# Kernel tuning notes

Hardware: AMD Instinct MI355X
Metric: run time of the kernel (lower is better)

Reference implementation:

```python
import jax, jax.numpy as jnp
import numpy as np

N_NODES = 50000
N_EDGES = 800000
IN_DIM = 256
HID = 128


def setup_inputs() -> dict:
    key = jax.random.key(0)
    ks = jax.random.split(key, 8)
    x = jax.random.normal(ks[0], (N_NODES, IN_DIM), dtype=jnp.float32)
    edge_index = jax.random.randint(ks[1], (2, N_EDGES), 0, N_NODES, dtype=jnp.int32)
    edge_weight = jax.random.uniform(ks[2], (N_EDGES,), dtype=jnp.float32)
    # xavier_normal with gain=1.414 as in torch init
    g = 1.414
    W1 = jax.random.normal(ks[3], (HID, IN_DIM), dtype=jnp.float32) * (g * np.sqrt(2.0 / (HID + IN_DIM)))
    W2 = jax.random.normal(ks[4], (HID, HID), dtype=jnp.float32) * (g * np.sqrt(2.0 / (HID + HID)))
    b1 = jnp.zeros((HID,), dtype=jnp.float32)
    b2 = jnp.zeros((HID,), dtype=jnp.float32)
    a1 = jnp.full((1,), 0.25, dtype=jnp.float32)  # nn.PReLU() default init
    a2 = jnp.full((1,), 0.25, dtype=jnp.float32)
    return {"x": x, "edge_index": edge_index, "edge_weight": edge_weight,
            "W1": W1, "b1": b1, "a1": a1, "W2": W2, "b2": b2, "a2": a2}


def _gcn_layer(z, W, b, a, src, dst, w):
    # linear (no bias): [N, out]
    fts = z @ W.T
    # spmm: out[dst] += w * fts[src]
    msg = fts[src] * w[:, None]                      # [E, out]
    out = jax.ops.segment_sum(msg, dst, num_segments=N_NODES) + b
    # PReLU (single shared parameter)
    return jnp.where(out >= 0, out, a * out)


def reference(x, edge_index, edge_weight, W1, b1, a1, W2, b2, a2):
    src, dst = edge_index[0], edge_index[1]
    z = _gcn_layer(x, W1, b1, a1, src, dst, edge_weight)
    z = _gcn_layer(z, W2, b2, a2, src, dst, edge_weight)
    return z
```

## Files before the change

kernel.cpp:

```cpp
#include <hip/hip_runtime.h>

#define HID 128
#define BSH 6
#define BSZ 64
#define NBMAX 1024

typedef unsigned int uint;
typedef unsigned short ushort;
typedef __attribute__((ext_vector_type(8))) short short8;
typedef __attribute__((ext_vector_type(4))) float f32x4;

__device__ __forceinline__ uint pack_bf16x2(float a, float b) {
    uint ua = __float_as_uint(a);
    ua += 0x7fffu + ((ua >> 16) & 1u);
    uint ub = __float_as_uint(b);
    ub += 0x7fffu + ((ub >> 16) & 1u);
    return (ua >> 16) | (ub & 0xffff0000u);
}

__device__ __forceinline__ ushort bf16_of(float x) {
    uint u = __float_as_uint(x);
    u += 0x7fffu + ((u >> 16) & 1u);
    return (ushort)(u >> 16);
}

__device__ __forceinline__ float4 addbias_prelu(float4 v, float4 b, float a) {
    v.x += b.x; v.y += b.y; v.z += b.z; v.w += b.w;
    v.x = v.x >= 0.f ? v.x : a * v.x;
    v.y = v.y >= 0.f ? v.y : a * v.y;
    v.z = v.z >= 0.f ? v.z : a * v.z;
    v.w = v.w >= 0.f ? v.w : a * v.w;
    return v;
}

union FragAB { uint4 u; short8 s; };

__global__ void w_to_frags(const float* __restrict__ W, ushort* __restrict__ Wb, int K) {
    int t = blockIdx.x * 256 + threadIdx.x;
    int total = (K / 32) * 8 * 64;
    if (t >= total) return;
    int lane = t & 63, f = t >> 6;
    int s = f >> 3, c = f & 7;
    int m = c * 16 + (lane & 15);
    int k0 = s * 32 + (lane >> 4) * 8;
    const float* wr = W + (size_t)m * K + k0;
    float4 a = *(const float4*)wr;
    float4 b = *(const float4*)(wr + 4);
    uint4 o = make_uint4(pack_bf16x2(a.x, a.y), pack_bf16x2(a.z, a.w),
                         pack_bf16x2(b.x, b.y), pack_bf16x2(b.z, b.w));
    *(uint4*)(Wb + (size_t)t * 8) = o;
}

template <int K, bool FUSE>
__global__ __launch_bounds__(256) void gemm_mfma(
    const float* __restrict__ X, const ushort* __restrict__ Wb,
    const float* __restrict__ bias, const float* __restrict__ alpha,
    ushort* __restrict__ out, int N) {
    const int lane = threadIdx.x & 63;
    const int wid  = threadIdx.x >> 6;
    const int n0   = blockIdx.x * 64 + wid * 16;
    const int arow = n0 + (lane & 15);
    const bool okA = arow < N;
    const int kgrp = (lane >> 4) * 8;
    const float* xrow = X + (size_t)arow * K;
    const float a_ = FUSE ? alpha[0] : 0.f;

    f32x4 acc[8];
#pragma unroll
    for (int c = 0; c < 8; ++c) acc[c] = (f32x4){0.f, 0.f, 0.f, 0.f};

#pragma unroll
    for (int s = 0; s < K / 32; ++s) {
        const int k0 = s * 32 + kgrp;
        float4 va = make_float4(0.f, 0.f, 0.f, 0.f), vb = va;
        if (okA) {
            va = *(const float4*)(xrow + k0);
            vb = *(const float4*)(xrow + k0 + 4);
        }
        if (FUSE) {
            float4 ba = *(const float4*)(bias + k0);
            float4 bb = *(const float4*)(bias + k0 + 4);
            va = addbias_prelu(va, ba, a_);
            vb = addbias_prelu(vb, bb, a_);
        }
        FragAB af;
        af.u = make_uint4(pack_bf16x2(va.x, va.y), pack_bf16x2(va.z, va.w),
                          pack_bf16x2(vb.x, vb.y), pack_bf16x2(vb.z, vb.w));
#pragma unroll
        for (int c = 0; c < 8; ++c) {
            FragAB bfr;
            bfr.u = *(const uint4*)(Wb + (size_t)((s * 8 + c) * 64 + lane) * 8);
            acc[c] = __builtin_amdgcn_mfma_f32_16x16x32_bf16(af.s, bfr.s, acc[c], 0, 0, 0);
        }
    }
    const int col = lane & 15;
    const int rbase = n0 + (lane >> 4) * 4;
#pragma unroll
    for (int c = 0; c < 8; ++c) {
#pragma unroll
        for (int r = 0; r < 4; ++r) {
            int n = rbase + r;
            if (n < N) out[(size_t)n * HID + c * 16 + col] = bf16_of(acc[c][r]);
        }
    }
}

__global__ __launch_bounds__(256) void bucket_hist(const int* __restrict__ dst,
                                                   int* __restrict__ ghist, int E, int NB) {
    __shared__ int h[NBMAX];
    for (int i = threadIdx.x; i < NB; i += 256) h[i] = 0;
    __syncthreads();
    int stride = gridDim.x * 256;
    for (int e = blockIdx.x * 256 + threadIdx.x; e < E; e += stride)
        atomicAdd(&h[dst[e] >> BSH], 1);
    __syncthreads();
    for (int i = threadIdx.x; i < NB; i += 256) {
        int c = h[i];
        if (c) atomicAdd(&ghist[i], c);
    }
}

__global__ __launch_bounds__(NBMAX) void bucket_scan(const int* __restrict__ ghist,
                                                     int* __restrict__ gbase,
                                                     int* __restrict__ gcur, int NB, int E) {
    __shared__ int l[NBMAX];
    int t = threadIdx.x;
    int v = (t < NB) ? ghist[t] : 0;
    l[t] = v;
    __syncthreads();
    int x = v;
    for (int o = 1; o < NBMAX; o <<= 1) {
        int y = (t >= o) ? l[t - o] : 0;
        __syncthreads();
        x += y;
        l[t] = x;
        __syncthreads();
    }
    if (t < NB) { gbase[t] = x - v; gcur[t] = x - v; }
    if (t == 0) gbase[NB] = E;
}

__global__ __launch_bounds__(256) void bucket_stage(
    const int* __restrict__ src, const int* __restrict__ dst,
    const float* __restrict__ w, int* __restrict__ gcur,
    int2* __restrict__ staged, int E, int NB) {
    __shared__ int lh[NBMAX], lb[NBMAX];
    for (int i = threadIdx.x; i < NB; i += 256) lh[i] = 0;
    __syncthreads();
    int chunk = (E + gridDim.x - 1) / gridDim.x;
    int c0 = blockIdx.x * chunk;
    int c1 = min(c0 + chunk, E);
    for (int e = c0 + threadIdx.x; e < c1; e += 256)
        atomicAdd(&lh[dst[e] >> BSH], 1);
    __syncthreads();
    for (int i = threadIdx.x; i < NB; i += 256) {
        int c = lh[i];
        lb[i] = c ? atomicAdd(&gcur[i], c) : 0;
        lh[i] = 0;
    }
    __syncthreads();
    for (int e = c0 + threadIdx.x; e < c1; e += 256) {
        int d = dst[e];
        int b = d >> BSH;
        int slot = lb[b] + atomicAdd(&lh[b], 1);
        staged[slot] = make_int2(src[e] | ((d & (BSZ - 1)) << 16), __float_as_int(w[e]));
    }
}

__global__ __launch_bounds__(256) void node_sort(
    const int* __restrict__ gbase, const int2* __restrict__ staged,
    int2* __restrict__ csr, int* __restrict__ off, int N) {
    __shared__ int hist[BSZ];
    __shared__ int cur[BSZ];
    const int b = blockIdx.x;
    const int s0 = gbase[b], s1 = gbase[b + 1];
    const int t = threadIdx.x;
    if (t < BSZ) hist[t] = 0;
    __syncthreads();
    for (int e = s0 + t; e < s1; e += 256)
        atomicAdd(&hist[(staged[e].x >> 16) & (BSZ - 1)], 1);
    __syncthreads();
    if (t < BSZ) {
        int x = hist[t];
        int incl = x;
#pragma unroll
        for (int o = 1; o < BSZ; o <<= 1) {
            int y = __shfl_up(incl, o, BSZ);
            if (t >= o) incl += y;
        }
        int excl = incl - x;
        cur[t] = excl;
        int n = (b << BSH) + t;
        if (n <= N) off[n] = s0 + excl;
    }
    __syncthreads();
    for (int e = s0 + t; e < s1; e += 256) {
        int2 m = staged[e];
        int d = (m.x >> 16) & (BSZ - 1);
        int p = atomicAdd(&cur[d], 1);
        csr[s0 + p] = m;
    }
}

__global__ __launch_bounds__(256) void csr_gather_bf16(
    const int* __restrict__ off, const int2* __restrict__ edges,
    const ushort* __restrict__ fts, float* __restrict__ out,
    const float* __restrict__ bias, const float* __restrict__ alpha, int N) {
    int d = blockIdx.x * 4 + (threadIdx.x >> 6);
    if (d >= N) return;
    int lane = threadIdx.x & 63;
    int p = off[d], end = off[d + 1];
    float acc0 = 0.f, acc1 = 0.f;

#define ROWU(e) (*((const uint*)(fts + (size_t)((e).x & 0xffff) * HID) + lane))
#define LO(r) __uint_as_float((r) << 16)
#define HI(r) __uint_as_float((r) & 0xffff0000u)

    for (; p + 3 < end; p += 4) {
        int2 e0 = edges[p], e1 = edges[p + 1], e2 = edges[p + 2], e3 = edges[p + 3];
        uint r0 = ROWU(e0), r1 = ROWU(e1), r2 = ROWU(e2), r3 = ROWU(e3);
        float w0 = __int_as_float(e0.y), w1 = __int_as_float(e1.y);
        float w2 = __int_as_float(e2.y), w3 = __int_as_float(e3.y);
        acc0 += w0 * LO(r0) + w1 * LO(r1) + w2 * LO(r2) + w3 * LO(r3);
        acc1 += w0 * HI(r0) + w1 * HI(r1) + w2 * HI(r2) + w3 * HI(r3);
    }
    for (; p < end; ++p) {
        int2 e = edges[p];
        uint r = ROWU(e);
        float wt = __int_as_float(e.y);
        acc0 += wt * LO(r);
        acc1 += wt * HI(r);
    }
#undef ROWU
#undef LO
#undef HI

    if (bias != nullptr) {
        float a = alpha[0];
        acc0 += bias[lane * 2 + 0];
        acc1 += bias[lane * 2 + 1];
        acc0 = acc0 >= 0.f ? acc0 : a * acc0;
        acc1 = acc1 >= 0.f ? acc1 : a * acc1;
    }
    *(float2*)&out[(size_t)d * HID + lane * 2] = make_float2(acc0, acc1);
}

extern "C" void kernel_launch(void* const* d_in, const int* in_sizes, int n_in,
                              void* d_out, int out_size, void* d_ws, size_t ws_size,
                              hipStream_t stream) {
    const float* x  = (const float*)d_in[0];
    const int*   ei = (const int*)d_in[1];
    const float* ew = (const float*)d_in[2];
    const float* W1 = (const float*)d_in[3];
    const float* b1 = (const float*)d_in[4];
    const float* a1 = (const float*)d_in[5];
    const float* W2 = (const float*)d_in[6];
    const float* b2 = (const float*)d_in[7];
    const float* a2 = (const float*)d_in[8];
    float* out = (float*)d_out;

    int N = in_sizes[0] / 256;
    int E = in_sizes[2];
    const int* src = ei;
    const int* dst = ei + E;
    int NB = (N + BSZ - 1) >> BSH;

    ushort* fts    = (ushort*)d_ws;
    int2*   staged = (int2*)(fts + (size_t)N * HID);
    int2*   csr    = staged + E;
    ushort* Wb1    = (ushort*)(csr + E);
    ushort* Wb2    = Wb1 + 128 * 256;
    int*    ghist  = (int*)(Wb2 + 128 * 128);
    int*    gbase  = ghist + NBMAX;
    int*    gcur   = gbase + NBMAX + 1;
    int*    off    = gcur + NBMAX;

    w_to_frags<<<16, 256, 0, stream>>>(W1, Wb1, 256);
    w_to_frags<<<8, 256, 0, stream>>>(W2, Wb2, 128);

    hipMemsetAsync(ghist, 0, NB * sizeof(int), stream);
    bucket_hist<<<256, 256, 0, stream>>>(dst, ghist, E, NB);
    bucket_scan<<<1, NBMAX, 0, stream>>>(ghist, gbase, gcur, NB, E);
    bucket_stage<<<256, 256, 0, stream>>>(src, dst, ew, gcur, staged, E, NB);
    node_sort<<<NB, 256, 0, stream>>>(gbase, staged, csr, off, N);

    int gblk = (N + 63) / 64;
    int ggrid = (N + 3) / 4;

    gemm_mfma<256, false><<<gblk, 256, 0, stream>>>(x, Wb1, nullptr, nullptr, fts, N);
    csr_gather_bf16<<<ggrid, 256, 0, stream>>>(off, csr, fts, out, nullptr, nullptr, N);

    gemm_mfma<128, true><<<gblk, 256, 0, stream>>>(out, Wb2, b1, a1, fts, N);
    csr_gather_bf16<<<ggrid, 256, 0, stream>>>(off, csr, fts, out, b2, a2, N);
}
```

Measured before the change: 170.3 us.

## Fuse layer-1 bias/PReLU into gather, emit bf16 intermediate, merge setup kernels

Layer-1 bias and PReLU now run at the end of the first CSR gather, which writes a bf16 intermediate instead of fp32. The second GEMM then loads bf16 A fragments directly, with no per-element conversion or bias work. The gather inner loop gains an 8-edge unrolled stage to keep more loads in flight. The two weight-conversion kernels and the histogram memset are merged into one launch, and the bucket_stage grid is halved. The cost is an extra bf16 rounding of the layer-1 activations and a larger workspace.

```diff
diff --git a/kernel.cpp b/kernel.cpp
--- a/kernel.cpp
+++ b/kernel.cpp
@@ -24,21 +24,20 @@
     return (ushort)(u >> 16);
 }
 
-__device__ __forceinline__ float4 addbias_prelu(float4 v, float4 b, float a) {
-    v.x += b.x; v.y += b.y; v.z += b.z; v.w += b.w;
-    v.x = v.x >= 0.f ? v.x : a * v.x;
-    v.y = v.y >= 0.f ? v.y : a * v.y;
-    v.z = v.z >= 0.f ? v.z : a * v.z;
-    v.w = v.w >= 0.f ? v.w : a * v.w;
-    return v;
-}
-
 union FragAB { uint4 u; short8 s; };
 
-__global__ void w_to_frags(const float* __restrict__ W, ushort* __restrict__ Wb, int K) {
-    int t = blockIdx.x * 256 + threadIdx.x;
-    int total = (K / 32) * 8 * 64;
-    if (t >= total) return;
+__global__ __launch_bounds__(256) void w_to_frags_both(
+    const float* __restrict__ W1, const float* __restrict__ W2,
+    ushort* __restrict__ Wb1, ushort* __restrict__ Wb2, int* __restrict__ ghist) {
+    int blk = blockIdx.x;
+    if (blk == 24) {
+        ((int4*)ghist)[threadIdx.x] = make_int4(0, 0, 0, 0);
+        return;
+    }
+    const float* W = (blk < 16) ? W1 : W2;
+    ushort* Wb = (blk < 16) ? Wb1 : Wb2;
+    int K = (blk < 16) ? 256 : 128;
+    int t = ((blk < 16) ? blk : blk - 16) * 256 + threadIdx.x;
     int lane = t & 63, f = t >> 6;
     int s = f >> 3, c = f & 7;
     int m = c * 16 + (lane & 15);
@@ -51,10 +50,9 @@
     *(uint4*)(Wb + (size_t)t * 8) = o;
 }
 
-template <int K, bool FUSE>
+template <int K, bool ABF16>
 __global__ __launch_bounds__(256) void gemm_mfma(
-    const float* __restrict__ X, const ushort* __restrict__ Wb,
-    const float* __restrict__ bias, const float* __restrict__ alpha,
+    const void* __restrict__ Xv, const ushort* __restrict__ Wb,
     ushort* __restrict__ out, int N) {
     const int lane = threadIdx.x & 63;
     const int wid  = threadIdx.x >> 6;
@@ -62,8 +60,8 @@
     const int arow = n0 + (lane & 15);
     const bool okA = arow < N;
     const int kgrp = (lane >> 4) * 8;
-    const float* xrow = X + (size_t)arow * K;
-    const float a_ = FUSE ? alpha[0] : 0.f;
+    const float*  xrow_f = (const float*)Xv + (size_t)arow * K;
+    const ushort* xrow_h = (const ushort*)Xv + (size_t)arow * K;
 
     f32x4 acc[8];
 #pragma unroll
@@ -72,20 +70,18 @@
 #pragma unroll
     for (int s = 0; s < K / 32; ++s) {
         const int k0 = s * 32 + kgrp;
-        float4 va = make_float4(0.f, 0.f, 0.f, 0.f), vb = va;
-        if (okA) {
-            va = *(const float4*)(xrow + k0);
-            vb = *(const float4*)(xrow + k0 + 4);
-        }
-        if (FUSE) {
-            float4 ba = *(const float4*)(bias + k0);
-            float4 bb = *(const float4*)(bias + k0 + 4);
-            va = addbias_prelu(va, ba, a_);
-            vb = addbias_prelu(vb, bb, a_);
-        }
         FragAB af;
-        af.u = make_uint4(pack_bf16x2(va.x, va.y), pack_bf16x2(va.z, va.w),
-                          pack_bf16x2(vb.x, vb.y), pack_bf16x2(vb.z, vb.w));
+        if (ABF16) {
+            af.u = okA ? *(const uint4*)(xrow_h + k0) : make_uint4(0, 0, 0, 0);
+        } else {
+            float4 va = make_float4(0.f, 0.f, 0.f, 0.f), vb = va;
+            if (okA) {
+                va = *(const float4*)(xrow_f + k0);
+                vb = *(const float4*)(xrow_f + k0 + 4);
+            }
+            af.u = make_uint4(pack_bf16x2(va.x, va.y), pack_bf16x2(va.z, va.w),
+                              pack_bf16x2(vb.x, vb.y), pack_bf16x2(vb.z, vb.w));
+        }
 #pragma unroll
         for (int c = 0; c < 8; ++c) {
             FragAB bfr;
@@ -202,9 +198,10 @@
     }
 }
 
+template <bool OUTBF16>
 __global__ __launch_bounds__(256) void csr_gather_bf16(
     const int* __restrict__ off, const int2* __restrict__ edges,
-    const ushort* __restrict__ fts, float* __restrict__ out,
+    const ushort* __restrict__ fts, void* __restrict__ outv,
     const float* __restrict__ bias, const float* __restrict__ alpha, int N) {
     int d = blockIdx.x * 4 + (threadIdx.x >> 6);
     if (d >= N) return;
@@ -216,6 +213,20 @@
 #define LO(r) __uint_as_float((r) << 16)
 #define HI(r) __uint_as_float((r) & 0xffff0000u)
 
+    for (; p + 7 < end; p += 8) {
+        int2 e[8];
+        uint r[8];
+#pragma unroll
+        for (int i = 0; i < 8; ++i) e[i] = edges[p + i];
+#pragma unroll
+        for (int i = 0; i < 8; ++i) r[i] = ROWU(e[i]);
+#pragma unroll
+        for (int i = 0; i < 8; ++i) {
+            float wt = __int_as_float(e[i].y);
+            acc0 += wt * LO(r[i]);
+            acc1 += wt * HI(r[i]);
+        }
+    }
     for (; p + 3 < end; p += 4) {
         int2 e0 = edges[p], e1 = edges[p + 1], e2 = edges[p + 2], e3 = edges[p + 3];
         uint r0 = ROWU(e0), r1 = ROWU(e1), r2 = ROWU(e2), r3 = ROWU(e3);
@@ -235,14 +246,16 @@
 #undef LO
 #undef HI
 
-    if (bias != nullptr) {
-        float a = alpha[0];
-        acc0 += bias[lane * 2 + 0];
-        acc1 += bias[lane * 2 + 1];
-        acc0 = acc0 >= 0.f ? acc0 : a * acc0;
-        acc1 = acc1 >= 0.f ? acc1 : a * acc1;
-    }
-    *(float2*)&out[(size_t)d * HID + lane * 2] = make_float2(acc0, acc1);
+    float a = alpha[0];
+    acc0 += bias[lane * 2 + 0];
+    acc1 += bias[lane * 2 + 1];
+    acc0 = acc0 >= 0.f ? acc0 : a * acc0;
+    acc1 = acc1 >= 0.f ? acc1 : a * acc1;
+    if (OUTBF16) {
+        ((uint*)outv)[(size_t)d * (HID / 2) + lane] = pack_bf16x2(acc0, acc1);
+    } else {
+        *(float2*)&((float*)outv)[(size_t)d * HID + lane * 2] = make_float2(acc0, acc1);
+    }
 }
 
 extern "C" void kernel_launch(void* const* d_in, const int* in_sizes, int n_in,
@@ -266,7 +279,8 @@
     int NB = (N + BSZ - 1) >> BSH;
 
     ushort* fts    = (ushort*)d_ws;
-    int2*   staged = (int2*)(fts + (size_t)N * HID);
+    ushort* agg    = fts + (size_t)N * HID;
+    int2*   staged = (int2*)(agg + (size_t)N * HID);
     int2*   csr    = staged + E;
     ushort* Wb1    = (ushort*)(csr + E);
     ushort* Wb2    = Wb1 + 128 * 256;
@@ -275,21 +289,19 @@
     int*    gcur   = gbase + NBMAX + 1;
     int*    off    = gcur + NBMAX;
 
-    w_to_frags<<<16, 256, 0, stream>>>(W1, Wb1, 256);
-    w_to_frags<<<8, 256, 0, stream>>>(W2, Wb2, 128);
-
-    hipMemsetAsync(ghist, 0, NB * sizeof(int), stream);
+    w_to_frags_both<<<25, 256, 0, stream>>>(W1, W2, Wb1, Wb2, ghist);
+
     bucket_hist<<<256, 256, 0, stream>>>(dst, ghist, E, NB);
     bucket_scan<<<1, NBMAX, 0, stream>>>(ghist, gbase, gcur, NB, E);
-    bucket_stage<<<256, 256, 0, stream>>>(src, dst, ew, gcur, staged, E, NB);
+    bucket_stage<<<128, 256, 0, stream>>>(src, dst, ew, gcur, staged, E, NB);
     node_sort<<<NB, 256, 0, stream>>>(gbase, staged, csr, off, N);
 
     int gblk = (N + 63) / 64;
     int ggrid = (N + 3) / 4;
 
-    gemm_mfma<256, false><<<gblk, 256, 0, stream>>>(x, Wb1, nullptr, nullptr, fts, N);
-    csr_gather_bf16<<<ggrid, 256, 0, stream>>>(off, csr, fts, out, nullptr, nullptr, N);
-
-    gemm_mfma<128, true><<<gblk, 256, 0, stream>>>(out, Wb2, b1, a1, fts, N);
-    csr_gather_bf16<<<ggrid, 256, 0, stream>>>(off, csr, fts, out, b2, a2, N);
-}
+    gemm_mfma<256, false><<<gblk, 256, 0, stream>>>(x, Wb1, fts, N);
+    csr_gather_bf16<true><<<ggrid, 256, 0, stream>>>(off, csr, fts, agg, b1, a1, N);
+
+    gemm_mfma<128, true><<<gblk, 256, 0, stream>>>(agg, Wb2, fts, N);
+    csr_gather_bf16<false><<<ggrid, 256, 0, stream>>>(off, csr, fts, out, b2, a2, N);
+}
```

Measured after the change: 157.6 us. 1.08x faster.
